# Optimization experiments

Measured on AMD Instinct MI355X. Metric: run time of the kernel, lower is better.

The kernel has to match this reference:

```python
import jax, jax.numpy as jnp
import numpy as np

T, B, D, H = 1024, 8, 1024, 16

def setup_inputs() -> dict:
    key = jax.random.key(0)
    ks = jax.random.split(key, 9)
    s = 0.02
    return {
        "x": jax.random.normal(ks[0], (T, B, D), dtype=jnp.float32),
        "Wq": jax.random.normal(ks[1], (D, D), dtype=jnp.float32) * s,
        "bq": jnp.zeros((D,), dtype=jnp.float32),
        "Wk": jax.random.normal(ks[2], (D, D), dtype=jnp.float32) * s,
        "bk": jnp.zeros((D,), dtype=jnp.float32),
        "Wv": jax.random.normal(ks[3], (D, D), dtype=jnp.float32) * s,
        "bv": jnp.zeros((D,), dtype=jnp.float32),
        "Wo": jax.random.normal(ks[4], (D, D), dtype=jnp.float32) * s,
        "bo": jnp.zeros((D,), dtype=jnp.float32),
        "n_heads": H,
    }

def reference(x, Wq, bq, Wk, bk, Wv, bv, Wo, bo, n_heads):
    t, b, D = x.shape
    h = n_heads
    d = D // h
    scale = 1.0 / jnp.sqrt(jnp.float32(d))
    # nn.Linear: y = x @ W.T + b
    q = (x @ Wq.T + bq).reshape(t, b, h, d)
    k = (x @ Wk.T + bk).reshape(t, b, h, d)
    v = (x @ Wv.T + bv).reshape(t, b, h, d)
    # scores: [b, h, t_query, t_key]
    scores = jnp.einsum('tbhd,sbhd->bhts', q, k) * scale
    attn = jax.nn.softmax(scores, axis=-1)
    out = jnp.einsum('bhts,sbhd->tbhd', attn, v).reshape(t, b, D)
    return out @ Wo.T + bo
```

## Files before the change

kernel.cpp:

```cpp
#include <hip/hip_runtime.h>


#define Tn 1024
#define Bn 8
#define Dn 1024
#define Hn 16
#define HDn 64
#define Mn 8192
#define Kn 1024

typedef float f32x4 __attribute__((ext_vector_type(4)));
typedef __bf16 bf16x8 __attribute__((ext_vector_type(8)));
typedef unsigned short u16x8 __attribute__((ext_vector_type(8)));
typedef unsigned short u16x4 __attribute__((ext_vector_type(4)));

#define GLL16(g, l)                                                        \
  __builtin_amdgcn_global_load_lds(                                        \
      (const __attribute__((address_space(1))) void*)(g),                  \
      (__attribute__((address_space(3))) void*)(l), 16, 0, 0)

__device__ __forceinline__ unsigned short f2bf(float f) {
  unsigned int u = __float_as_uint(f);
  u += 0x7fffu + ((u >> 16) & 1u);
  return (unsigned short)(u >> 16);
}

__global__ __launch_bounds__(256) void cvt_kernel(
    const float* __restrict__ src, unsigned short* __restrict__ dst, int n4) {
  int i = blockIdx.x * 256 + threadIdx.x;
  const int stride = gridDim.x * 256;
  for (; i < n4; i += stride) {
    const float4 v = ((const float4*)src)[i];
    u16x4 o;
    o.x = f2bf(v.x); o.y = f2bf(v.y); o.z = f2bf(v.z); o.w = f2bf(v.w);
    ((u16x4*)dst)[i] = o;
  }
}

__global__ __launch_bounds__(256) void cvt4_kernel(
    const float* __restrict__ s0, const float* __restrict__ s1,
    const float* __restrict__ s2, const float* __restrict__ s3,
    unsigned short* __restrict__ d0, unsigned short* __restrict__ d1,
    unsigned short* __restrict__ d2, unsigned short* __restrict__ d3, int n4) {
  const int z = blockIdx.z;
  const float* src = (z == 0) ? s0 : (z == 1) ? s1 : (z == 2) ? s2 : s3;
  unsigned short* dst = (z == 0) ? d0 : (z == 1) ? d1 : (z == 2) ? d2 : d3;
  int i = blockIdx.x * 256 + threadIdx.x;
  const int stride = gridDim.x * 256;
  for (; i < n4; i += stride) {
    const float4 v = ((const float4*)src)[i];
    u16x4 o;
    o.x = f2bf(v.x); o.y = f2bf(v.y); o.z = f2bf(v.z); o.w = f2bf(v.w);
    ((u16x4*)dst)[i] = o;
  }
}

__device__ __forceinline__ void gemm128_core(
    const unsigned short* __restrict__ A, const unsigned short* __restrict__ Bw,
    unsigned short* lds_a, unsigned short* lds_b, int bm, int bn,
    f32x4 acc[4][4]) {
  const int tid = threadIdx.x;
  const int lane = tid & 63;
  const int w = tid >> 6;
  const int wr = w >> 1, wc = w & 1;
  const int fr = lane & 15, fg = lane >> 4;

  const int p0 = tid, p1 = tid + 256;
  const int r0 = p0 >> 2, c0 = (p0 & 3) ^ ((r0 ^ (r0 >> 2)) & 3);
  const int r1 = p1 >> 2, c1 = (p1 & 3) ^ ((r1 ^ (r1 >> 2)) & 3);
  const unsigned short* gA0 = A + (size_t)(bm * 128 + r0) * Kn + c0 * 8;
  const unsigned short* gA1 = A + (size_t)(bm * 128 + r1) * Kn + c1 * 8;
  const unsigned short* gB0 = Bw + (size_t)(bn * 128 + r0) * Kn + c0 * 8;
  const unsigned short* gB1 = Bw + (size_t)(bn * 128 + r1) * Kn + c1 * 8;

  int aoff[4], boff[4];
#pragma unroll
  for (int m = 0; m < 4; m++) {
    const int row = wr * 64 + m * 16 + fr;
    aoff[m] = row * 32 + ((fg ^ ((row ^ (row >> 2)) & 3)) * 8);
  }
#pragma unroll
  for (int n = 0; n < 4; n++) {
    const int row = wc * 64 + n * 16 + fr;
    boff[n] = row * 32 + ((fg ^ ((row ^ (row >> 2)) & 3)) * 8);
  }

  for (int k0 = 0; k0 < Kn; k0 += 32) {
    GLL16(gA0 + k0, &lds_a[tid * 8]);
    GLL16(gA1 + k0, &lds_a[(tid + 256) * 8]);
    GLL16(gB0 + k0, &lds_b[tid * 8]);
    GLL16(gB1 + k0, &lds_b[(tid + 256) * 8]);
    __syncthreads();
    bf16x8 af[4], bfr[4];
#pragma unroll
    for (int m = 0; m < 4; m++) af[m] = *(const bf16x8*)&lds_a[aoff[m]];
#pragma unroll
    for (int n = 0; n < 4; n++) bfr[n] = *(const bf16x8*)&lds_b[boff[n]];
#pragma unroll
    for (int m = 0; m < 4; m++)
#pragma unroll
      for (int n = 0; n < 4; n++)
        acc[m][n] = __builtin_amdgcn_mfma_f32_16x16x32_bf16(af[m], bfr[n],
                                                            acc[m][n], 0, 0, 0);
    __syncthreads();
  }
}

__global__ __launch_bounds__(256) void gemm_qkv(
    const unsigned short* __restrict__ xbf, const unsigned short* __restrict__ wq,
    const unsigned short* __restrict__ wk, const unsigned short* __restrict__ wv,
    const float* __restrict__ bq, const float* __restrict__ bk,
    const float* __restrict__ bv, unsigned short* __restrict__ qd,
    unsigned short* __restrict__ kd, unsigned short* __restrict__ vd) {
  __shared__ __align__(16) unsigned short lds_a[128 * 32];
  __shared__ __align__(16) unsigned short lds_b[128 * 32];
  const int z = blockIdx.z;
  const unsigned short* Bw = (z == 0) ? wq : (z == 1) ? wk : wv;
  const float* bias = (z == 0) ? bq : (z == 1) ? bk : bv;
  unsigned short* dst = (z == 0) ? qd : (z == 1) ? kd : vd;
  const float sc = (z == 0) ? 0.125f * 1.44269504088896f : 1.0f;

  f32x4 acc[4][4] = {};
  gemm128_core(xbf, Bw, lds_a, lds_b, blockIdx.x, blockIdx.y, acc);

  const int tid = threadIdx.x, lane = tid & 63, w = tid >> 6;
  const int wr = w >> 1, wc = w & 1, fr = lane & 15, fg = lane >> 4;
#pragma unroll
  for (int n = 0; n < 4; n++) {
    const int gcol = blockIdx.y * 128 + wc * 64 + n * 16 + fr;
    const float bc = bias[gcol];
    const int hh = gcol >> 6, dd = gcol & 63;
#pragma unroll
    for (int m = 0; m < 4; m++) {
      const int rowbase = blockIdx.x * 128 + wr * 64 + m * 16 + fg * 4;
#pragma unroll
      for (int r = 0; r < 4; r++) {
        const int grow = rowbase + r;
        const int tt = grow >> 3, bb = grow & 7;
        const float v = (acc[m][n][r] + bc) * sc;
        dst[((size_t)(bb * Hn + hh) * Tn + tt) * HDn + dd] = f2bf(v);
      }
    }
  }
}

__global__ __launch_bounds__(256) void gemm_out(
    const unsigned short* __restrict__ abf, const unsigned short* __restrict__ wo,
    const float* __restrict__ bo, float* __restrict__ out) {
  __shared__ __align__(16) unsigned short lds_a[128 * 32];
  __shared__ __align__(16) unsigned short lds_b[128 * 32];
  f32x4 acc[4][4] = {};
  gemm128_core(abf, wo, lds_a, lds_b, blockIdx.x, blockIdx.y, acc);

  const int tid = threadIdx.x, lane = tid & 63, w = tid >> 6;
  const int wr = w >> 1, wc = w & 1, fr = lane & 15, fg = lane >> 4;
#pragma unroll
  for (int n = 0; n < 4; n++) {
    const int gcol = blockIdx.y * 128 + wc * 64 + n * 16 + fr;
    const float bc = bo[gcol];
#pragma unroll
    for (int m = 0; m < 4; m++) {
      const int rowbase = blockIdx.x * 128 + wr * 64 + m * 16 + fg * 4;
#pragma unroll
      for (int r = 0; r < 4; r++) {
        const int grow = rowbase + r;
        out[(size_t)grow * Dn + gcol] = acc[m][n][r] + bc;
      }
    }
  }
}

__global__ __launch_bounds__(256) void transpose_v(
    const unsigned short* __restrict__ src, unsigned short* __restrict__ dst) {
  __shared__ unsigned short tile[64][72];
  const int tid = threadIdx.x;
  const size_t base = (size_t)blockIdx.y * ((size_t)Tn * HDn);
  const int t0 = blockIdx.x * 64;
#pragma unroll
  for (int it = 0; it < 2; it++) {
    const int p = it * 256 + tid;
    const int r = p >> 3, c = (p & 7) * 8;
    *(u16x8*)&tile[r][c] =
        *(const u16x8*)(src + base + (size_t)(t0 + r) * HDn + c);
  }
  __syncthreads();
#pragma unroll
  for (int it = 0; it < 2; it++) {
    const int p = it * 256 + tid;
    const int d = p >> 3, tc = (p & 7) * 8;
    u16x8 v;
#pragma unroll
    for (int j = 0; j < 8; j++) v[j] = tile[tc + j][d];
    *(u16x8*)(dst + base + (size_t)d * Tn + t0 + tc) = v;
  }
}

__global__ __launch_bounds__(256) void attn_fwd(
    const unsigned short* __restrict__ Q, const unsigned short* __restrict__ K,
    const unsigned short* __restrict__ Vt, unsigned short* __restrict__ Ob) {
  __shared__ __align__(16) unsigned short k2[2][64 * 64];
  __shared__ __align__(16) unsigned short v2[2][64 * 64];
  __shared__ __align__(16) unsigned short p_all[64 * 64];

  const int tid = threadIdx.x, lane = tid & 63, w = tid >> 6;
  const int fr = lane & 15, fg = lane >> 4;
  const int qt = blockIdx.x;
  const int bh = blockIdx.y;
  const int bb = bh >> 4, hh = bh & 15;

  const unsigned short* Qbh = Q + (size_t)bh * (Tn * HDn);
  const unsigned short* Kbh = K + (size_t)bh * (Tn * HDn);
  const unsigned short* Vbh = Vt + (size_t)bh * (HDn * Tn);

  const int p0 = tid, p1 = tid + 256;
  const int r0 = p0 >> 3, c0 = (p0 & 7) ^ (r0 & 7);
  const int r1 = p1 >> 3, c1 = (p1 & 7) ^ (r1 & 7);

  GLL16(Qbh + (size_t)(qt * 64 + r0) * HDn + c0 * 8, &p_all[p0 * 8]);
  GLL16(Qbh + (size_t)(qt * 64 + r1) * HDn + c1 * 8, &p_all[p1 * 8]);
  __syncthreads();
  bf16x8 qa[2];
#pragma unroll
  for (int ks = 0; ks < 2; ks++) {
    const int row = w * 16 + fr;
    const int blk = (ks * 4 + fg) ^ (row & 7);
    qa[ks] = *(const bf16x8*)&p_all[row * 64 + blk * 8];
  }

#define STAGE_KV(nx, bi)                                                     \
  do {                                                                       \
    GLL16(Kbh + (size_t)((nx) * 64 + r0) * HDn + c0 * 8, &k2[bi][p0 * 8]);   \
    GLL16(Kbh + (size_t)((nx) * 64 + r1) * HDn + c1 * 8, &k2[bi][p1 * 8]);   \
    GLL16(Vbh + (size_t)r0 * Tn + (nx) * 64 + c0 * 8, &v2[bi][p0 * 8]);      \
    GLL16(Vbh + (size_t)r1 * Tn + (nx) * 64 + c1 * 8, &v2[bi][p1 * 8]);      \
  } while (0)

  STAGE_KV(0, 0);
  __syncthreads();

  f32x4 o[4] = {};
  float mrow[4] = {-1e30f, -1e30f, -1e30f, -1e30f};
  float lsum[4] = {};
  unsigned short* pl = &p_all[w * 1024];

  for (int kt = 0; kt < 16; kt++) {
    const int cur = kt & 1;
    if (kt < 15) STAGE_KV(kt + 1, cur ^ 1);
    const unsigned short* kl = k2[cur];
    const unsigned short* vl = v2[cur];

    f32x4 s[4] = {};
    __builtin_amdgcn_s_setprio(1);
#pragma unroll
    for (int n = 0; n < 4; n++) {
#pragma unroll
      for (int ks = 0; ks < 2; ks++) {
        const int krow = n * 16 + fr;
        const int blk = (ks * 4 + fg) ^ (krow & 7);
        const bf16x8 kb = *(const bf16x8*)&kl[krow * 64 + blk * 8];
        s[n] = __builtin_amdgcn_mfma_f32_16x16x32_bf16(qa[ks], kb, s[n], 0, 0, 0);
      }
    }
    __builtin_amdgcn_s_setprio(0);

    float esc[4];
#pragma unroll
    for (int r = 0; r < 4; r++) {
      float tm = fmaxf(fmaxf(s[0][r], s[1][r]), fmaxf(s[2][r], s[3][r]));
      tm = fmaxf(tm, __shfl_xor(tm, 1));
      tm = fmaxf(tm, __shfl_xor(tm, 2));
      tm = fmaxf(tm, __shfl_xor(tm, 4));
      tm = fmaxf(tm, __shfl_xor(tm, 8));
      const float mn = fmaxf(mrow[r], tm);
      esc[r] = exp2f(mrow[r] - mn);
      mrow[r] = mn;
    }
    float rs[4] = {};
#pragma unroll
    for (int n = 0; n < 4; n++)
#pragma unroll
      for (int r = 0; r < 4; r++) {
        const float p = exp2f(s[n][r] - mrow[r]);
        s[n][r] = p;
        rs[r] += p;
      }
#pragma unroll
    for (int r = 0; r < 4; r++) {
      rs[r] += __shfl_xor(rs[r], 1);
      rs[r] += __shfl_xor(rs[r], 2);
      rs[r] += __shfl_xor(rs[r], 4);
      rs[r] += __shfl_xor(rs[r], 8);
      lsum[r] = lsum[r] * esc[r] + rs[r];
    }
#pragma unroll
    for (int n = 0; n < 4; n++)
#pragma unroll
      for (int r = 0; r < 4; r++) o[n][r] *= esc[r];

#pragma unroll
    for (int n = 0; n < 4; n++)
#pragma unroll
      for (int r = 0; r < 4; r++) {
        const int prow = fg * 4 + r;
        const int pcol = n * 16 + fr;
        pl[prow * 64 + (((pcol >> 3) ^ (prow & 7)) * 8) + (pcol & 7)] =
            f2bf(s[n][r]);
      }

    __builtin_amdgcn_s_setprio(1);
#pragma unroll
    for (int ks = 0; ks < 2; ks++) {
      const int ablk = (ks * 4 + fg) ^ (fr & 7);
      const bf16x8 pa = *(const bf16x8*)&pl[fr * 64 + ablk * 8];
#pragma unroll
      for (int n = 0; n < 4; n++) {
        const int vrow = n * 16 + fr;
        const int vblk = (ks * 4 + fg) ^ (vrow & 7);
        const bf16x8 vb = *(const bf16x8*)&vl[vrow * 64 + vblk * 8];
        o[n] = __builtin_amdgcn_mfma_f32_16x16x32_bf16(pa, vb, o[n], 0, 0, 0);
      }
    }
    __builtin_amdgcn_s_setprio(0);
    __syncthreads();
  }
#undef STAGE_KV

#pragma unroll
  for (int r = 0; r < 4; r++) lsum[r] = 1.0f / lsum[r];
  const int tbase = qt * 64 + w * 16 + fg * 4;
#pragma unroll
  for (int n = 0; n < 4; n++) {
    const int dcol = n * 16 + fr;
#pragma unroll
    for (int r = 0; r < 4; r++) {
      const int tt = tbase + r;
      const float val = o[n][r] * lsum[r];
      Ob[((size_t)(tt * Bn + bb)) * Dn + hh * HDn + dcol] = f2bf(val);
    }
  }
}

extern "C" void kernel_launch(void* const* d_in, const int* in_sizes, int n_in,
                              void* d_out, int out_size, void* d_ws,
                              size_t ws_size, hipStream_t stream) {
  (void)in_sizes; (void)n_in; (void)out_size; (void)ws_size;
  const float* x  = (const float*)d_in[0];
  const float* Wq = (const float*)d_in[1];
  const float* bq = (const float*)d_in[2];
  const float* Wk = (const float*)d_in[3];
  const float* bk = (const float*)d_in[4];
  const float* Wv = (const float*)d_in[5];
  const float* bv = (const float*)d_in[6];
  const float* Wo = (const float*)d_in[7];
  const float* bo = (const float*)d_in[8];
  float* out = (float*)d_out;

  unsigned short* ws  = (unsigned short*)d_ws;
  unsigned short* xbf = ws;
  unsigned short* wqb = xbf + (size_t)Mn * Kn;
  unsigned short* wkb = wqb + (size_t)Dn * Dn;
  unsigned short* wvb = wkb + (size_t)Dn * Dn;
  unsigned short* wob = wvb + (size_t)Dn * Dn;
  unsigned short* qb  = wob + (size_t)Dn * Dn;
  unsigned short* kb  = qb + (size_t)Mn * Dn;
  unsigned short* vb  = kb + (size_t)Mn * Dn;
  unsigned short* vtb = xbf;
  unsigned short* ab  = vb;

  cvt_kernel<<<1024, 256, 0, stream>>>(x, xbf, Mn * Kn / 4);
  cvt4_kernel<<<dim3(256, 1, 4), 256, 0, stream>>>(
      Wq, Wk, Wv, Wo, wqb, wkb, wvb, wob, Dn * Dn / 4);

  gemm_qkv<<<dim3(Mn / 128, Dn / 128, 3), 256, 0, stream>>>(
      xbf, wqb, wkb, wvb, bq, bk, bv, qb, kb, vb);
  transpose_v<<<dim3(Tn / 64, Bn * Hn), 256, 0, stream>>>(vb, vtb);
  attn_fwd<<<dim3(Tn / 64, Bn * Hn), 256, 0, stream>>>(qb, kb, vtb, ab);
  gemm_out<<<dim3(Mn / 128, Dn / 128), 256, 0, stream>>>(ab, wob, bo, out);
}
```

Before: 312.7 us.

## Use lazy softmax rescale, MFMA row sums, and native bf16 conversion in attention

The attention loop now rescales the running max, row sum and output accumulator only when some row's tile max exceeds the stored max by more than a threshold (wave-uniform branch via __any). This removes most per-tile exp and multiply work. Row sums are computed with two extra MFMAs against a vector of ones instead of a shuffle-reduction tree, and the manual bf16 rounding is replaced by the native __bf16 conversion. The trade-off is that unnormalized probabilities can reach up to 2^8, and the row sums are taken from bf16-rounded values, which slightly changes accuracy.

```diff
diff --git a/kernel.cpp b/kernel.cpp
--- a/kernel.cpp
+++ b/kernel.cpp
@@ -23,6 +23,11 @@
   unsigned int u = __float_as_uint(f);
   u += 0x7fffu + ((u >> 16) & 1u);
   return (unsigned short)(u >> 16);
+}
+
+__device__ __forceinline__ unsigned short bfbits(float f) {
+  __bf16 h = (__bf16)f;
+  return __builtin_bit_cast(unsigned short, h);
 }
 
 __global__ __launch_bounds__(256) void cvt_kernel(
@@ -227,6 +232,10 @@
     qa[ks] = *(const bf16x8*)&p_all[row * 64 + blk * 8];
   }
 
+  bf16x8 vones;
+#pragma unroll
+  for (int j = 0; j < 8; j++) vones[j] = (__bf16)1.0f;
+
 #define STAGE_KV(nx, bi)                                                     \
   do {                                                                       \
     GLL16(Kbh + (size_t)((nx) * 64 + r0) * HDn + c0 * 8, &k2[bi][p0 * 8]);   \
@@ -263,39 +272,30 @@
     }
     __builtin_amdgcn_s_setprio(0);
 
-    float esc[4];
+    float tm[4];
 #pragma unroll
     for (int r = 0; r < 4; r++) {
-      float tm = fmaxf(fmaxf(s[0][r], s[1][r]), fmaxf(s[2][r], s[3][r]));
-      tm = fmaxf(tm, __shfl_xor(tm, 1));
-      tm = fmaxf(tm, __shfl_xor(tm, 2));
-      tm = fmaxf(tm, __shfl_xor(tm, 4));
-      tm = fmaxf(tm, __shfl_xor(tm, 8));
-      const float mn = fmaxf(mrow[r], tm);
-      esc[r] = exp2f(mrow[r] - mn);
-      mrow[r] = mn;
-    }
-    float rs[4] = {};
-#pragma unroll
-    for (int n = 0; n < 4; n++)
+      float t = fmaxf(fmaxf(s[0][r], s[1][r]), fmaxf(s[2][r], s[3][r]));
+      t = fmaxf(t, __shfl_xor(t, 1));
+      t = fmaxf(t, __shfl_xor(t, 2));
+      t = fmaxf(t, __shfl_xor(t, 4));
+      t = fmaxf(t, __shfl_xor(t, 8));
+      tm[r] = t;
+    }
+
+    const int grew = (tm[0] > mrow[0] + 8.0f) | (tm[1] > mrow[1] + 8.0f) |
+                     (tm[2] > mrow[2] + 8.0f) | (tm[3] > mrow[3] + 8.0f);
+    if (__any(grew)) {
 #pragma unroll
       for (int r = 0; r < 4; r++) {
-        const float p = exp2f(s[n][r] - mrow[r]);
-        s[n][r] = p;
-        rs[r] += p;
-      }
-#pragma unroll
-    for (int r = 0; r < 4; r++) {
-      rs[r] += __shfl_xor(rs[r], 1);
-      rs[r] += __shfl_xor(rs[r], 2);
-      rs[r] += __shfl_xor(rs[r], 4);
-      rs[r] += __shfl_xor(rs[r], 8);
-      lsum[r] = lsum[r] * esc[r] + rs[r];
-    }
-#pragma unroll
-    for (int n = 0; n < 4; n++)
-#pragma unroll
-      for (int r = 0; r < 4; r++) o[n][r] *= esc[r];
+        const float mn = fmaxf(mrow[r], tm[r]);
+        const float esc = exp2f(mrow[r] - mn);
+        mrow[r] = mn;
+        lsum[r] *= esc;
+#pragma unroll
+        for (int n = 0; n < 4; n++) o[n][r] *= esc;
+      }
+    }
 
 #pragma unroll
     for (int n = 0; n < 4; n++)
@@ -304,20 +304,30 @@
         const int prow = fg * 4 + r;
         const int pcol = n * 16 + fr;
         pl[prow * 64 + (((pcol >> 3) ^ (prow & 7)) * 8) + (pcol & 7)] =
-            f2bf(s[n][r]);
-      }
-
-    __builtin_amdgcn_s_setprio(1);
+            bfbits(exp2f(s[n][r] - mrow[r]));
+      }
+
+    bf16x8 pa[2];
 #pragma unroll
     for (int ks = 0; ks < 2; ks++) {
       const int ablk = (ks * 4 + fg) ^ (fr & 7);
-      const bf16x8 pa = *(const bf16x8*)&pl[fr * 64 + ablk * 8];
+      pa[ks] = *(const bf16x8*)&pl[fr * 64 + ablk * 8];
+    }
+    f32x4 ssum = {};
+    ssum = __builtin_amdgcn_mfma_f32_16x16x32_bf16(pa[0], vones, ssum, 0, 0, 0);
+    ssum = __builtin_amdgcn_mfma_f32_16x16x32_bf16(pa[1], vones, ssum, 0, 0, 0);
+#pragma unroll
+    for (int r = 0; r < 4; r++) lsum[r] += ssum[r];
+
+    __builtin_amdgcn_s_setprio(1);
+#pragma unroll
+    for (int ks = 0; ks < 2; ks++) {
 #pragma unroll
       for (int n = 0; n < 4; n++) {
         const int vrow = n * 16 + fr;
         const int vblk = (ks * 4 + fg) ^ (vrow & 7);
         const bf16x8 vb = *(const bf16x8*)&vl[vrow * 64 + vblk * 8];
-        o[n] = __builtin_amdgcn_mfma_f32_16x16x32_bf16(pa, vb, o[n], 0, 0, 0);
+        o[n] = __builtin_amdgcn_mfma_f32_16x16x32_bf16(pa[ks], vb, o[n], 0, 0, 0);
       }
     }
     __builtin_amdgcn_s_setprio(0);
@@ -335,7 +345,7 @@
     for (int r = 0; r < 4; r++) {
       const int tt = tbase + r;
       const float val = o[n][r] * lsum[r];
-      Ob[((size_t)(tt * Bn + bb)) * Dn + hh * HDn + dcol] = f2bf(val);
+      Ob[((size_t)(tt * Bn + bb)) * Dn + hh * HDn + dcol] = bfbits(val);
     }
   }
 }
```

Result: faster. 289.0 us (-7.6%).
